# Kernel tuning notes

Measured on AMD Instinct MI355X. Metric: run time of the kernel, lower is better.

Reference implementation:

```python
import jax, jax.numpy as jnp
import numpy as np

MARGIN = 0.0
GAP = 0.4
N, D, C = 8192, 128, 10


def setup_inputs() -> dict:
    key = jax.random.key(0)
    k1, k2, k3 = jax.random.split(key, 3)
    inputs = jax.random.normal(k1, (N, D), dtype=jnp.float32)
    pred = jax.random.normal(k2, (N, C), dtype=jnp.float32)
    targets = jax.random.randint(k3, (N,), 0, C, dtype=jnp.int64)
    return {"inputs": inputs, "pred": pred, "targets": targets}


def reference(inputs, pred, targets):
    n = inputs.shape[0]
    # pairwise euclidean distances: ||xi||^2 + ||xj||^2 - 2 xi.xj, clamped + sqrt
    sq = jnp.sum(inputs * inputs, axis=1)                      # [n]
    dist = sq[:, None] + sq[None, :] - 2.0 * (inputs @ inputs.T)
    dist = jnp.sqrt(jnp.clip(dist, 1e-12))                     # [n, n]
    same = targets[:, None] == targets[None, :]                # [n, n] bool

    # confusion detection (original runs under no_grad)
    p = jax.nn.softmax(jax.lax.stop_gradient(pred), axis=1)
    val, top2 = jax.lax.top_k(p, 2)                            # [n,2]
    confuse = (val[:, 0] - val[:, 1] <= GAP) | (top2[:, 0] != targets)  # [n]

    # hard mining per row: hardest positive (max over same-class), hardest negative (min over diff-class)
    dist_ap = jnp.max(jnp.where(same, dist, -jnp.inf), axis=1)  # [n]
    dist_an = jnp.min(jnp.where(same, jnp.inf, dist), axis=1)   # [n]

    # MarginRankingLoss(margin=MARGIN) with y=1: mean(relu(-(an - ap) + margin)) over confused rows
    per_row = jnp.maximum(dist_ap - dist_an + MARGIN, 0.0)
    cnt = jnp.sum(confuse.astype(jnp.float32))
    loss = jnp.sum(jnp.where(confuse, per_row, 0.0)) / jnp.maximum(cnt, 1.0)
    return jnp.where(cnt > 0, loss, 0.0)
```

## Files before the change

kernel.cpp:

```cpp
#include <hip/hip_runtime.h>

#define NROWS 8192
#define DIMX  128
#define DIM2  160
#define NCLS  10
#define GAPV  0.4f
#define BIAS  2048.0f
#define C0    128.0f
#define CHUNK 512
#define NCHUNK (NROWS / CHUNK)
#define NRG    (NROWS / 256)
#define SLAB  64
#define NSLAB (CHUNK / SLAB)
#define LDST  168

typedef __attribute__((ext_vector_type(8))) short bf16x8;
typedef __attribute__((ext_vector_type(4))) float f32x4;

__device__ __forceinline__ unsigned fenc(float f) {
  unsigned u = __float_as_uint(f);
  return (u & 0x80000000u) ? ~u : (u | 0x80000000u);
}
__device__ __forceinline__ float fdec(unsigned u) {
  return (u & 0x80000000u) ? __uint_as_float(u & 0x7fffffffu) : __uint_as_float(~u);
}
__device__ __forceinline__ short f2bf(float f) {
  unsigned u = __float_as_uint(f);
  u += 0x7fffu + ((u >> 16) & 1u);
  return (short)(u >> 16);
}

__global__ __launch_bounds__(256) void prep_k(const float* __restrict__ x,
                                              const int* __restrict__ tgt,
                                              const float* __restrict__ pred,
                                              short* __restrict__ xa,
                                              short* __restrict__ xbm,
                                              float* __restrict__ sq,
                                              unsigned* __restrict__ emax,
                                              unsigned* __restrict__ emin,
                                              int* __restrict__ conf,
                                              unsigned* __restrict__ ctrs) {
  if (blockIdx.x == 0 && threadIdx.x < NRG + 3) ctrs[threadIdx.x] = 0u;

  const int wave = threadIdx.x >> 6;
  const int lane = threadIdx.x & 63;
  const int row  = blockIdx.x * 4 + wave;
  const float* p = x + (size_t)row * DIMX;
  const float a = p[lane];
  const float b = p[lane + 64];
  float s = a * a + b * b;
  #pragma unroll
  for (int m = 1; m < 64; m <<= 1) s += __shfl_xor(s, m, 64);

  short* pa = xa  + (size_t)row * DIM2;
  short* pb = xbm + (size_t)row * DIM2;
  pa[lane] = f2bf(a); pa[lane + 64] = f2bf(b);
  pb[lane] = f2bf(a); pb[lane + 64] = f2bf(b);

  const int cls = tgt[row];
  if (lane < 32) {
    short va, vb;
    if (lane == 0)          { va = (short)0x3F80; vb = f2bf(-0.5f * (s - C0)); }
    else if (lane <= NCLS)  { const bool hit = (lane - 1) == cls;
                              va = hit ? (short)0x4200 : (short)0;
                              vb = hit ? (short)0xC200 : (short)0; }
    else                    { va = 0; vb = 0; }
    pa[128 + lane] = va;
    pb[128 + lane] = vb;
  }

  if (lane == 0) {
    sq[row]   = s;
    emax[row] = fenc(-INFINITY);
    emin[row] = fenc(INFINITY);
    const float* pp = pred + (size_t)row * NCLS;
    float v[NCLS];
    #pragma unroll
    for (int c = 0; c < NCLS; ++c) v[c] = pp[c];
    float m1 = v[0]; int i1 = 0;
    #pragma unroll
    for (int c = 1; c < NCLS; ++c)
      if (v[c] > m1) { m1 = v[c]; i1 = c; }
    float m2 = -INFINITY, sum = 0.f;
    #pragma unroll
    for (int c = 0; c < NCLS; ++c) {
      sum += __expf(v[c] - m1);
      if (c != i1) m2 = fmaxf(m2, v[c]);
    }
    const float d01 = (1.f - __expf(m2 - m1)) / sum;
    conf[row] = (d01 <= GAPV) || (i1 != cls);
  }
}

__global__ __launch_bounds__(256, 2) void gram_k(const short* __restrict__ xa,
                                                 const short* __restrict__ xbm,
                                                 const float* __restrict__ sq,
                                                 const int* __restrict__ conf,
                                                 unsigned* __restrict__ emax,
                                                 unsigned* __restrict__ emin,
                                                 unsigned* __restrict__ ctrs,
                                                 float* __restrict__ out) {
  __shared__ short lds[2][SLAB * LDST];
  __shared__ float red[2][4];
  __shared__ int   flag;
  const int tid  = threadIdx.x;
  const int wave = tid >> 6;
  const int lane = tid & 63;
  const int quad = lane >> 4;
  const int m16  = lane & 15;
  const int i0    = blockIdx.x * 256 + wave * 64;
  const int jbase = blockIdx.y * CHUNK;

  unsigned* rg_done = ctrs;
  unsigned* g_done  = ctrs + NRG;
  float*    Ssum    = (float*)(ctrs + NRG + 1);
  float*    Csum    = (float*)(ctrs + NRG + 2);

  bf16x8 A[4][5];
  #pragma unroll
  for (int r = 0; r < 4; ++r) {
    const short* pa = xa + (size_t)(i0 + r * 16 + m16) * DIM2 + quad * 8;
    #pragma unroll
    for (int ks = 0; ks < 5; ++ks)
      A[r][ks] = *(const bf16x8*)(pa + ks * 32);
  }
  #pragma unroll
  for (int r = 0; r < 4; ++r)
    #pragma unroll
    for (int ks = 0; ks < 5; ++ks)
      asm volatile("" : "+v"(A[r][ks]));

  float gmin[4][4], gmax[4][4];
  #pragma unroll
  for (int r = 0; r < 4; ++r)
    #pragma unroll
    for (int q = 0; q < 4; ++q) { gmin[r][q] = INFINITY; gmax[r][q] = -INFINITY; }

  const int scol = tid >> 2;
  const int s16  = tid & 3;
  const short* gsrc = xbm + (size_t)(jbase + scol) * DIM2 + s16 * 8;
  short* ldst = (short*)lds + scol * LDST + s16 * 8;

  {
    uint4 st[5];
    #pragma unroll
    for (int u = 0; u < 5; ++u) st[u] = *(const uint4*)(gsrc + u * 32);
    #pragma unroll
    for (int u = 0; u < 5; ++u) *(uint4*)(ldst + u * 32) = st[u];
  }
  __syncthreads();

  for (int s = 0; s < NSLAB; ++s) {
    const int snext = (s + 1) & (NSLAB - 1);
    const short* gn = gsrc + (size_t)snext * SLAB * DIM2;
    uint4 nx[5];
    #pragma unroll
    for (int u = 0; u < 5; ++u) nx[u] = *(const uint4*)(gn + u * 32);

    const short* buf = lds[s & 1];
    #pragma unroll
    for (int jt = 0; jt < SLAB / 16; ++jt) {
      const short* pb = buf + (jt * 16 + m16) * LDST + quad * 8;
      bf16x8 B[5];
      #pragma unroll
      for (int ks = 0; ks < 5; ++ks) B[ks] = *(const bf16x8*)(pb + ks * 32);

      f32x4 acc[4];
      #pragma unroll
      for (int r = 0; r < 4; ++r) acc[r] = (f32x4){0.f, 0.f, 0.f, 0.f};
      #pragma unroll
      for (int ks = 0; ks < 5; ++ks)
        #pragma unroll
        for (int r = 0; r < 4; ++r)
          acc[r] = __builtin_amdgcn_mfma_f32_16x16x32_bf16(A[r][ks], B[ks], acc[r], 0, 0, 0);

      #pragma unroll
      for (int r = 0; r < 4; ++r)
        #pragma unroll
        for (int q = 0; q < 4; ++q) {
          gmin[r][q] = fminf(gmin[r][q], acc[r][q]);
          gmax[r][q] = fmaxf(gmax[r][q], acc[r][q]);
        }
    }

    short* dst = (short*)lds + ((s + 1) & 1) * (SLAB * LDST) + scol * LDST + s16 * 8;
    #pragma unroll
    for (int u = 0; u < 5; ++u) *(uint4*)(dst + u * 32) = nx[u];
    __syncthreads();
  }

  #pragma unroll
  for (int m = 1; m <= 8; m <<= 1)
    #pragma unroll
    for (int r = 0; r < 4; ++r)
      #pragma unroll
      for (int q = 0; q < 4; ++q) {
        gmin[r][q] = fminf(gmin[r][q], __shfl_xor(gmin[r][q], m, 64));
        gmax[r][q] = fmaxf(gmax[r][q], __shfl_xor(gmax[r][q], m, 64));
      }

  if (m16 == 0) {
    #pragma unroll
    for (int r = 0; r < 4; ++r)
      #pragma unroll
      for (int q = 0; q < 4; ++q) {
        const int row = i0 + r * 16 + quad * 4 + q;
        atomicMax(&emax[row], fenc(C0 - 2.f * gmin[r][q] - BIAS));
        atomicMin(&emin[row], fenc(C0 - 2.f * gmax[r][q]));
      }
  }

  __syncthreads();
  if (tid == 0) {
    __threadfence();
    flag = (atomicAdd(&rg_done[blockIdx.x], 1u) == NCHUNK - 1u);
  }
  __syncthreads();
  if (!flag) return;

  const int row = blockIdx.x * 256 + tid;
  float ps = 0.f, pc = 0.f;
  if (conf[row]) {
    const float hi = fdec(atomicMax(&emax[row], 0u));
    const float lo = fdec(atomicMin(&emin[row], 0xFFFFFFFFu));
    const float ap = sqrtf(fmaxf(sq[row] + hi, 1e-12f));
    const float an = sqrtf(fmaxf(sq[row] + lo, 1e-12f));
    ps = fmaxf(ap - an, 0.f);
    pc = 1.f;
  }
  #pragma unroll
  for (int m = 1; m < 64; m <<= 1) {
    ps += __shfl_xor(ps, m, 64);
    pc += __shfl_xor(pc, m, 64);
  }
  if (lane == 0) { red[0][wave] = ps; red[1][wave] = pc; }
  __syncthreads();
  if (tid == 0) {
    float S = red[0][0] + red[0][1] + red[0][2] + red[0][3];
    float C = red[1][0] + red[1][1] + red[1][2] + red[1][3];
    atomicAdd(Ssum, S);
    atomicAdd(Csum, C);
    __threadfence();
    if (atomicAdd(g_done, 1u) == NRG - 1u) {
      const float St = atomicAdd(Ssum, 0.f);
      const float Ct = atomicAdd(Csum, 0.f);
      out[0] = (Ct > 0.f) ? (St / fmaxf(Ct, 1.f)) : 0.f;
    }
  }
}

extern "C" void kernel_launch(void* const* d_in, const int* in_sizes, int n_in,
                              void* d_out, int out_size, void* d_ws, size_t ws_size,
                              hipStream_t stream) {
  const float* x    = (const float*)d_in[0];
  const float* pred = (const float*)d_in[1];
  const int*   tgt  = (const int*)d_in[2];
  float* out = (float*)d_out;

  char* w = (char*)d_ws;
  const size_t arr_bytes = (size_t)NROWS * DIM2 * 2;
  short*    xa   = (short*)w;
  short*    xbm  = (short*)(w + arr_bytes);
  float*    sq   = (float*)(w + 2 * arr_bytes);
  unsigned* emax = (unsigned*)(w + 2 * arr_bytes + (size_t)NROWS * 4);
  unsigned* emin = (unsigned*)(w + 2 * arr_bytes + (size_t)NROWS * 8);
  int*      conf = (int*)(w + 2 * arr_bytes + (size_t)NROWS * 12);
  unsigned* ctrs = (unsigned*)(w + 2 * arr_bytes + (size_t)NROWS * 16);

  hipLaunchKernelGGL(prep_k, dim3(NROWS / 4), dim3(256), 0, stream,
                     x, tgt, pred, xa, xbm, sq, emax, emin, conf, ctrs);
  hipLaunchKernelGGL(gram_k, dim3(NRG, NCHUNK), dim3(256), 0, stream,
                     xa, xbm, sq, conf, emax, emin, ctrs, out);
}
```

Measured before the change: 95.60 us.

## Load B tiles directly from global into registers, drop LDS staging

Removes the shared-memory double-buffered slab staging of the column operand. Each wave now loads its B fragments straight from global memory (L2-resident) into a 4-deep rotating register ring, prefetching two tiles ahead. This eliminates LDS writes, LDS reads and block-wide barriers, but every wave loads B redundantly, which raises global/L2 traffic fourfold and adds register pressure. It also relaxes the asm barrier on A and adds a threadfence before the final reduction.

```diff
diff --git a/kernel.cpp b/kernel.cpp
--- a/kernel.cpp
+++ b/kernel.cpp
@@ -7,12 +7,11 @@
 #define GAPV  0.4f
 #define BIAS  2048.0f
 #define C0    128.0f
+#define RGR   256
+#define NRG   (NROWS / RGR)
 #define CHUNK 512
 #define NCHUNK (NROWS / CHUNK)
-#define NRG    (NROWS / 256)
-#define SLAB  64
-#define NSLAB (CHUNK / SLAB)
-#define LDST  168
+#define NJ    (CHUNK / 16)
 
 typedef __attribute__((ext_vector_type(8))) short bf16x8;
 typedef __attribute__((ext_vector_type(4))) float f32x4;
@@ -100,7 +99,6 @@
                                                  unsigned* __restrict__ emin,
                                                  unsigned* __restrict__ ctrs,
                                                  float* __restrict__ out) {
-  __shared__ short lds[2][SLAB * LDST];
   __shared__ float red[2][4];
   __shared__ int   flag;
   const int tid  = threadIdx.x;
@@ -108,7 +106,7 @@
   const int lane = tid & 63;
   const int quad = lane >> 4;
   const int m16  = lane & 15;
-  const int i0    = blockIdx.x * 256 + wave * 64;
+  const int i0    = blockIdx.x * RGR + wave * 64;
   const int jbase = blockIdx.y * CHUNK;
 
   unsigned* rg_done = ctrs;
@@ -128,7 +126,7 @@
   for (int r = 0; r < 4; ++r)
     #pragma unroll
     for (int ks = 0; ks < 5; ++ks)
-      asm volatile("" : "+v"(A[r][ks]));
+      asm("" : "+v"(A[r][ks]));
 
   float gmin[4][4], gmax[4][4];
   #pragma unroll
@@ -136,34 +134,24 @@
     #pragma unroll
     for (int q = 0; q < 4; ++q) { gmin[r][q] = INFINITY; gmax[r][q] = -INFINITY; }
 
-  const int scol = tid >> 2;
-  const int s16  = tid & 3;
-  const short* gsrc = xbm + (size_t)(jbase + scol) * DIM2 + s16 * 8;
-  short* ldst = (short*)lds + scol * LDST + s16 * 8;
-
-  {
-    uint4 st[5];
-    #pragma unroll
-    for (int u = 0; u < 5; ++u) st[u] = *(const uint4*)(gsrc + u * 32);
-    #pragma unroll
-    for (int u = 0; u < 5; ++u) *(uint4*)(ldst + u * 32) = st[u];
-  }
-  __syncthreads();
-
-  for (int s = 0; s < NSLAB; ++s) {
-    const int snext = (s + 1) & (NSLAB - 1);
-    const short* gn = gsrc + (size_t)snext * SLAB * DIM2;
-    uint4 nx[5];
-    #pragma unroll
-    for (int u = 0; u < 5; ++u) nx[u] = *(const uint4*)(gn + u * 32);
-
-    const short* buf = lds[s & 1];
-    #pragma unroll
-    for (int jt = 0; jt < SLAB / 16; ++jt) {
-      const short* pb = buf + (jt * 16 + m16) * LDST + quad * 8;
-      bf16x8 B[5];
-      #pragma unroll
-      for (int ks = 0; ks < 5; ++ks) B[ks] = *(const bf16x8*)(pb + ks * 32);
+  const short* pb0 = xbm + (size_t)(jbase + m16) * DIM2 + quad * 8;
+
+  bf16x8 B[4][5];
+  #pragma unroll
+  for (int t = 0; t < 2; ++t) {
+    const short* pl = pb0 + (size_t)t * 16 * DIM2;
+    #pragma unroll
+    for (int u = 0; u < 5; ++u) B[t][u] = *(const bf16x8*)(pl + u * 32);
+  }
+
+  for (int jt = 0; jt < NJ; jt += 4) {
+    #pragma unroll
+    for (int t = 0; t < 4; ++t) {
+      const int j2 = (jt + t + 2) & (NJ - 1);
+      const short* pl = pb0 + (size_t)j2 * 16 * DIM2;
+      #pragma unroll
+      for (int u = 0; u < 5; ++u)
+        B[(t + 2) & 3][u] = *(const bf16x8*)(pl + u * 32);
 
       f32x4 acc[4];
       #pragma unroll
@@ -172,7 +160,7 @@
       for (int ks = 0; ks < 5; ++ks)
         #pragma unroll
         for (int r = 0; r < 4; ++r)
-          acc[r] = __builtin_amdgcn_mfma_f32_16x16x32_bf16(A[r][ks], B[ks], acc[r], 0, 0, 0);
+          acc[r] = __builtin_amdgcn_mfma_f32_16x16x32_bf16(A[r][ks], B[t][ks], acc[r], 0, 0, 0);
 
       #pragma unroll
       for (int r = 0; r < 4; ++r)
@@ -182,11 +170,6 @@
           gmax[r][q] = fmaxf(gmax[r][q], acc[r][q]);
         }
     }
-
-    short* dst = (short*)lds + ((s + 1) & 1) * (SLAB * LDST) + scol * LDST + s16 * 8;
-    #pragma unroll
-    for (int u = 0; u < 5; ++u) *(uint4*)(dst + u * 32) = nx[u];
-    __syncthreads();
   }
 
   #pragma unroll
@@ -217,8 +200,9 @@
   }
   __syncthreads();
   if (!flag) return;
-
-  const int row = blockIdx.x * 256 + tid;
+  __threadfence();
+
+  const int row = blockIdx.x * RGR + tid;
   float ps = 0.f, pc = 0.f;
   if (conf[row]) {
     const float hi = fdec(atomicMax(&emax[row], 0u));
```

Result: slower. 107.1 us (+12.0%).
